# Optimization experiments

Measured on AMD Instinct MI355X. Metric: run time of the kernel, lower is better.

## Reference

```python
import jax, jax.numpy as jnp
import numpy as np

V, S, D, NL, DF, R, DG = 50257, 1024, 640, 16, 2560, 24, 256
PLU = R * (R - 1) // 2  # 276
OFFSETS = (1, 2, 4, 8, 16, 32, 64)
EPS = 1e-6
LN_EPS = 1e-5
II, JJ = np.triu_indices(R, k=1)  # matches torch.triu_indices(r, r, offset=1) ordering


def setup_inputs() -> dict:
    key = jax.random.key(0)
    ks = jax.random.split(key, 16)
    B, L = 4, 1024
    def n(k, shape):
        return jax.random.normal(k, shape, jnp.float32) * 0.02
    return {
        "input_ids": jax.random.randint(ks[0], (B, L), 0, V, jnp.int32),
        "tok_emb": n(ks[1], (V, D)),          # tied with lm_head
        "pos_emb": n(ks[2], (S, D)),
        "ln1_w": jnp.ones((NL, D)), "ln1_b": jnp.zeros((NL, D)),
        "red_w": n(ks[3], (NL, R, D)), "red_b": jnp.zeros((NL, R)),
        "gp1_w": n(ks[4], (NL, DG, PLU)), "gp1_b": jnp.zeros((NL, DG)),
        "gp2_w": n(ks[5], (NL, D, DG)), "gp2_b": jnp.zeros((NL, D)),
        "gate_w": n(ks[6], (NL, D, 2 * D)), "gate_b": jnp.zeros((NL, D)),
        "ln2_w": jnp.ones((NL, D)), "ln2_b": jnp.zeros((NL, D)),
        "fc1_w": n(ks[7], (NL, DF, D)), "fc1_b": jnp.zeros((NL, DF)),
        "fc2_w": n(ks[8], (NL, D, DF)), "fc2_b": jnp.zeros((NL, D)),
        "fn_w": jnp.ones((D,)), "fn_b": jnp.zeros((D,)),
    }


def _ln(x, w, b):
    m = jnp.mean(x, -1, keepdims=True)
    v = jnp.mean((x - m) ** 2, -1, keepdims=True)
    return (x - m) / jnp.sqrt(v + LN_EPS) * w + b


def _forward(input_ids, tok_emb, pos_emb, ln1_w, ln1_b, red_w, red_b,
             gp1_w, gp1_b, gp2_w, gp2_b, gate_w, gate_b,
             ln2_w, ln2_b, fc1_w, fc1_b, fc2_w, fc2_b, fn_w, fn_b):
    B, L = input_ids.shape
    x = tok_emb[input_ids] + pos_emb[jnp.arange(L)][None]  # (B,L,D), dropout=0 (eval)
    for l in range(NL):
        # --- CausalGrassmannMixer ---
        h = _ln(x, ln1_w[l], ln1_b[l])
        z = jnp.einsum('bld,rd->blr', h, red_w[l]) + red_b[l]  # (B,L,R)
        geom_sum = jnp.zeros_like(h)
        count = jnp.zeros((B, L, 1), h.dtype)
        for delta in OFFSETS:
            if delta >= L:
                continue
            z_past = jnp.pad(z[:, :L - delta], ((0, 0), (delta, 0), (0, 0)))
            # Plucker coordinates, normalized
            p = z_past[..., II] * z[..., JJ] - z_past[..., JJ] * z[..., II]  # (B,L,PLU)
            norm = jnp.maximum(jnp.sqrt(jnp.sum(p * p, -1, keepdims=True)), EPS)
            p = p / norm
            g = jax.nn.gelu(jnp.einsum('blp,gp->blg', p, gp1_w[l]) + gp1_b[l], approximate=False)
            g = jnp.einsum('blg,dg->bld', g, gp2_w[l]) + gp2_b[l]
            mask = (jnp.arange(L) >= delta).astype(h.dtype)[None, :, None]
            geom_sum = geom_sum + g * mask
            count = count + mask
        g = geom_sum / jnp.maximum(count, 1.0)
        alpha = jax.nn.sigmoid(
            jnp.einsum('ble,de->bld', jnp.concatenate([h, g], -1), gate_w[l]) + gate_b[l])
        x = x + alpha * h + (1.0 - alpha) * g
        # --- FeedForward ---
        h2 = _ln(x, ln2_w[l], ln2_b[l])
        ff = jax.nn.gelu(jnp.einsum('bld,fd->blf', h2, fc1_w[l]) + fc1_b[l], approximate=False)
        x = x + jnp.einsum('blf,df->bld', ff, fc2_w[l]) + fc2_b[l]
    x = _ln(x, fn_w, fn_b)
    return jnp.einsum('bld,vd->blv', x, tok_emb)  # tied lm_head


def reference(input_ids, tok_emb, pos_emb, ln1_w, ln1_b, red_w, red_b,
              gp1_w, gp1_b, gp2_w, gp2_b, gate_w, gate_b,
              ln2_w, ln2_b, fc1_w, fc1_b, fc2_w, fc2_b, fn_w, fn_b):
    return _forward(input_ids, tok_emb, pos_emb, ln1_w, ln1_b, red_w, red_b,
                    gp1_w, gp1_b, gp2_w, gp2_b, gate_w, gate_b,
                    ln2_w, ln2_b, fc1_w, fc1_b, fc2_w, fc2_b, fn_w, fn_b)
```

## Files before the change

kernel.cpp:

```cpp
#include <hip/hip_runtime.h>
#include <cmath>

#define V_ 50257
#define D_ 640
#define NL_ 16
#define DF_ 2560
#define R_ 24
#define DG_ 256
#define PLU_ 276
#define PLUP_ 288
#define B_ 4
#define L_ 1024
#define M_ (B_*L_)
#define EPS_ 1e-6f
#define LN_EPS_ 1e-5f

typedef __bf16 bf16x8 __attribute__((ext_vector_type(8)));
typedef float f32x4 __attribute__((ext_vector_type(4)));

__device__ __forceinline__ float gelu_exact(float x) {
    return 0.5f * x * (1.0f + erff(x * 0.70710678118654752f));
}
__device__ __forceinline__ float sigmoid_f(float x) {
    return 1.0f / (1.0f + expf(-x));
}
__device__ __forceinline__ ushort f2b(float f) {
    union { float f; unsigned u; } v; v.f = f;
    unsigned u = v.u;
    return (ushort)((u + 0x7FFFu + ((u >> 16) & 1u)) >> 16);
}
__device__ __forceinline__ float b2f(ushort b) {
    union { unsigned u; float f; } v; v.u = ((unsigned)b) << 16;
    return v.f;
}

#define GLOAD16(gptr, lptr) \
    __builtin_amdgcn_global_load_lds((const __attribute__((address_space(1))) void*)(gptr), \
                                     (__attribute__((address_space(3))) void*)(lptr), 16, 0, 0)


#define AS_(b) (shmem + (b) * 4096)
#define BS_(b) (shmem + 8192 + (b) * 4096)
#define STAGE128(b, k0) do { \
    GLOAD16(A + (size_t)(bm + w * 32 + srow) * (size_t)K + ((k0) + scol), AS_(b) + (w * 32) * 32); \
    GLOAD16(A + (size_t)(bm + w * 32 + 16 + srow) * (size_t)K + ((k0) + scol), AS_(b) + (w * 32 + 16) * 32); \
    int rb0_ = bn + w * 32 + srow;      if (rb0_ > N - 1) rb0_ = N - 1; \
    int rb1_ = bn + w * 32 + 16 + srow; if (rb1_ > N - 1) rb1_ = N - 1; \
    GLOAD16(W + (size_t)rb0_ * (size_t)K + ((k0) + scol), BS_(b) + (w * 32) * 32); \
    GLOAD16(W + (size_t)rb1_ * (size_t)K + ((k0) + scol), BS_(b) + (w * 32 + 16) * 32); \
} while (0)

template<int EPI>
__global__ __launch_bounds__(256) void mgemm128_k(
    const ushort* __restrict__ A, const ushort* __restrict__ W,
    const float* __restrict__ bias, float* __restrict__ Cf,
    ushort* __restrict__ Cb, int M, int N, int K)
{
    __shared__ ushort shmem[16384];
    const int tid = threadIdx.x;
    const int lane = tid & 63;
    const int w = tid >> 6;
    const int wr = w >> 1, wc = w & 1;
    const int lr = lane & 15, lk = lane >> 4;
    const int bm = blockIdx.x * 128, bn = blockIdx.y * 128;
    const int srow = lane >> 2;
    const int scol = (((lane & 3) ^ ((srow >> 1) & 3)) * 8);

    f32x4 acc[4][4] = {};
    const int nt = K >> 5;

    STAGE128(0, 0);
    asm volatile("s_waitcnt vmcnt(0)" ::: "memory");
    __builtin_amdgcn_s_barrier();

    int cur = 0;
    for (int t = 0; t < nt; ++t) {
        if (t + 1 < nt) { STAGE128(cur ^ 1, (t + 1) * 32); }
        bf16x8 af[4], bfr[4];
        #pragma unroll
        for (int m = 0; m < 4; ++m) {
            int rr = wr * 64 + m * 16 + lr;
            af[m] = *reinterpret_cast<const bf16x8*>(&AS_(cur)[rr * 32 + ((lk ^ ((rr >> 1) & 3)) * 8)]);
        }
        #pragma unroll
        for (int n = 0; n < 4; ++n) {
            int rr = wc * 64 + n * 16 + lr;
            bfr[n] = *reinterpret_cast<const bf16x8*>(&BS_(cur)[rr * 32 + ((lk ^ ((rr >> 1) & 3)) * 8)]);
        }
        #pragma unroll
        for (int m = 0; m < 4; ++m)
            #pragma unroll
            for (int n = 0; n < 4; ++n)
                acc[m][n] = __builtin_amdgcn_mfma_f32_16x16x32_bf16(af[m], bfr[n], acc[m][n], 0, 0, 0);
        asm volatile("s_waitcnt vmcnt(0)" ::: "memory");
        __builtin_amdgcn_s_barrier();
        cur ^= 1;
    }

    #pragma unroll
    for (int n = 0; n < 4; ++n) {
        int col = bn + wc * 64 + n * 16 + lr;
        if (col >= N) continue;
        float bsv = bias ? bias[col] : 0.0f;
        #pragma unroll
        for (int m = 0; m < 4; ++m) {
            #pragma unroll
            for (int r4 = 0; r4 < 4; ++r4) {
                int row = bm + wr * 64 + m * 16 + lk * 4 + r4;
                float o = acc[m][n][r4] + bsv;
                size_t idx = (size_t)row * N + col;
                if (EPI == 1) Cb[idx] = f2b(gelu_exact(o));
                else          Cb[idx] = f2b(o);
            }
        }
    }
}

#define AS2_(b) (shmem + (b) * 8192)
#define BS2_(b) (shmem + 16384 + (b) * 4096)
#define STAGE256(b, k0) do { \
    GLOAD16(A + (size_t)(bm + w * 32 + srow) * (size_t)K + ((k0) + scol), AS2_(b) + (w * 32) * 32); \
    GLOAD16(A + (size_t)(bm + w * 32 + 16 + srow) * (size_t)K + ((k0) + scol), AS2_(b) + (w * 32 + 16) * 32); \
    int rb_ = bn + w * 16 + srow; if (rb_ > N - 1) rb_ = N - 1; \
    GLOAD16(W + (size_t)rb_ * (size_t)K + ((k0) + scol), BS2_(b) + (w * 16) * 32); \
} while (0)

__global__ __launch_bounds__(512) void mgemm256nt_k(
    const ushort* __restrict__ A, const ushort* __restrict__ W,
    float* __restrict__ Cf, int M, int N, int K)
{
    __shared__ ushort shmem[24576];
    const int tid = threadIdx.x;
    const int lane = tid & 63;
    const int w = tid >> 6;
    const int wr = w >> 1, wc = w & 1;
    const int lr = lane & 15, lk = lane >> 4;
    const int bm = blockIdx.x * 256, bn = blockIdx.y * 128;
    const int srow = lane >> 2;
    const int scol = (((lane & 3) ^ ((srow >> 1) & 3)) * 8);

    f32x4 acc[4][4] = {};
    const int nt = K >> 5;

    STAGE256(0, 0);
    asm volatile("s_waitcnt vmcnt(0)" ::: "memory");
    __builtin_amdgcn_s_barrier();

    int cur = 0;
    for (int t = 0; t < nt; ++t) {
        if (t + 1 < nt) { STAGE256(cur ^ 1, (t + 1) * 32); }
        bf16x8 af[4], bfr[4];
        #pragma unroll
        for (int m = 0; m < 4; ++m) {
            int rr = wr * 64 + m * 16 + lr;
            af[m] = *reinterpret_cast<const bf16x8*>(&AS2_(cur)[rr * 32 + ((lk ^ ((rr >> 1) & 3)) * 8)]);
        }
        #pragma unroll
        for (int n = 0; n < 4; ++n) {
            int rr = wc * 64 + n * 16 + lr;
            bfr[n] = *reinterpret_cast<const bf16x8*>(&BS2_(cur)[rr * 32 + ((lk ^ ((rr >> 1) & 3)) * 8)]);
        }
        #pragma unroll
        for (int m = 0; m < 4; ++m)
            #pragma unroll
            for (int n = 0; n < 4; ++n)
                acc[m][n] = __builtin_amdgcn_mfma_f32_16x16x32_bf16(af[m], bfr[n], acc[m][n], 0, 0, 0);
        asm volatile("s_waitcnt vmcnt(0)" ::: "memory");
        __builtin_amdgcn_s_barrier();
        cur ^= 1;
    }

    float* lds_f = (float*)shmem;
    const int wbase = w * (16 * 68);
    #pragma unroll
    for (int m = 0; m < 4; ++m) {
        #pragma unroll
        for (int n = 0; n < 4; ++n) {
            #pragma unroll
            for (int r4 = 0; r4 < 4; ++r4)
                lds_f[wbase + (lk * 4 + r4) * 68 + n * 16 + lr] = acc[m][n][r4];
        }
        __syncthreads();
        #pragma unroll
        for (int r = 0; r < 16; ++r) {
            int row = bm + wr * 64 + m * 16 + r;
            int col = bn + wc * 64 + lane;
            float v = lds_f[wbase + r * 68 + lane];
            if (col < N)
                __builtin_nontemporal_store(v, &Cf[(size_t)row * N + col]);
        }
        __syncthreads();
    }
}

#define STAGE12864(b, k0) do { \
    GLOAD16(A + (size_t)(bm + w * 16 + srow) * (size_t)K + ((k0) + scol), &As[b][(w * 16) * 32]); \
    GLOAD16(A + (size_t)(bm + 64 + w * 16 + srow) * (size_t)K + ((k0) + scol), &As[b][(64 + w * 16) * 32]); \
    GLOAD16(W + (size_t)(bn + w * 16 + srow) * (size_t)K + ((k0) + scol), &Bs[b][(w * 16) * 32]); \
} while (0)

template<int EPI>
__global__ __launch_bounds__(256) void mgemm12864_k(
    const ushort* __restrict__ A, const ushort* __restrict__ W,
    const float* __restrict__ bias, float* __restrict__ Cf,
    const ushort* __restrict__ hg, ushort* __restrict__ ub,
    int M, int N, int K)
{
    __shared__ ushort As[2][128 * 32];
    __shared__ ushort Bs[2][64 * 32];
    const int tid = threadIdx.x;
    const int lane = tid & 63;
    const int w = tid >> 6;
    const int wr = w >> 1, wc = w & 1;
    const int lr = lane & 15, lk = lane >> 4;
    const int bm = blockIdx.x * 128, bn = blockIdx.y * 64;
    const int srow = lane >> 2;
    const int scol = (((lane & 3) ^ ((srow >> 1) & 3)) * 8);

    f32x4 acc[4][2] = {};
    const int nt = K >> 5;

    STAGE12864(0, 0);
    asm volatile("s_waitcnt vmcnt(0)" ::: "memory");
    __builtin_amdgcn_s_barrier();

    int cur = 0;
    for (int t = 0; t < nt; ++t) {
        if (t + 1 < nt) { STAGE12864(cur ^ 1, (t + 1) * 32); }
        bf16x8 af[4], bfr[2];
        #pragma unroll
        for (int m = 0; m < 4; ++m) {
            int rr = wr * 64 + m * 16 + lr;
            af[m] = *reinterpret_cast<const bf16x8*>(&As[cur][rr * 32 + ((lk ^ ((rr >> 1) & 3)) * 8)]);
        }
        #pragma unroll
        for (int n = 0; n < 2; ++n) {
            int rr = wc * 32 + n * 16 + lr;
            bfr[n] = *reinterpret_cast<const bf16x8*>(&Bs[cur][rr * 32 + ((lk ^ ((rr >> 1) & 3)) * 8)]);
        }
        #pragma unroll
        for (int m = 0; m < 4; ++m)
            #pragma unroll
            for (int n = 0; n < 2; ++n)
                acc[m][n] = __builtin_amdgcn_mfma_f32_16x16x32_bf16(af[m], bfr[n], acc[m][n], 0, 0, 0);
        asm volatile("s_waitcnt vmcnt(0)" ::: "memory");
        __builtin_amdgcn_s_barrier();
        cur ^= 1;
    }

    #pragma unroll
    for (int n = 0; n < 2; ++n) {
        int col = bn + wc * 32 + n * 16 + lr;
        float bsv = bias ? bias[col] : 0.0f;
        #pragma unroll
        for (int m = 0; m < 4; ++m) {
            #pragma unroll
            for (int r4 = 0; r4 < 4; ++r4) {
                int row = bm + wr * 64 + m * 16 + lk * 4 + r4;
                float o = acc[m][n][r4] + bsv;
                size_t idx = (size_t)row * N + col;
                if (EPI == 2) {
                    float a = sigmoid_f(o);
                    float hv = b2f(hg[(size_t)row * (2 * D_) + col]);
                    float gv = b2f(hg[(size_t)row * (2 * D_) + D_ + col]);
                    Cf[idx] = Cf[idx] + a * hv + (1.0f - a) * gv;
                } else if (EPI == 3) {
                    Cf[idx] += o;
                } else if (EPI == 5) {
                    if ((row & (L_ - 1)) == 0) o = 0.0f;
                    ub[(size_t)row * (2 * D_) + D_ + col] = f2b(o);
                }
            }
        }
    }
}

__global__ __launch_bounds__(256) void credsum_k(
    const ushort* __restrict__ c1b, ushort* __restrict__ crb)
{
    int idx4 = blockIdx.x * 256 + threadIdx.x;
    if (idx4 >= M_ * DG_ / 4) return;
    int idx = idx4 * 4;
    int row = idx / DG_;
    int l = row & (L_ - 1);
    float s0 = 0.f, s1 = 0.f, s2 = 0.f, s3 = 0.f;
    int c = 0;
    #pragma unroll
    for (int oi = 0; oi < 7; ++oi) {
        if (l >= (1 << oi)) {
            ushort4 v = *reinterpret_cast<const ushort4*>(c1b + (size_t)oi * M_ * DG_ + idx);
            s0 += b2f(v.x); s1 += b2f(v.y); s2 += b2f(v.z); s3 += b2f(v.w);
            ++c;
        }
    }
    float inv = 1.0f / (float)max(c, 1);
    ushort4 o;
    o.x = f2b(s0 * inv); o.y = f2b(s1 * inv); o.z = f2b(s2 * inv); o.w = f2b(s3 * inv);
    *reinterpret_cast<ushort4*>(crb + idx) = o;
}

__global__ __launch_bounds__(128) void lnred_k(
    const float* __restrict__ x, const float* __restrict__ w,
    const float* __restrict__ b, const float* __restrict__ rw,
    const float* __restrict__ rb, ushort* __restrict__ hgb,
    float* __restrict__ z)
{
    int row = blockIdx.x;
    int tid = threadIdx.x;
    const float* xr = x + (size_t)row * D_;
    __shared__ float hrow[D_];
    __shared__ float parts[R_][5];
    float v[5];
    float sum = 0.f, sumsq = 0.f;
    #pragma unroll
    for (int t = 0; t < 5; ++t) {
        v[t] = xr[tid + t * 128];
        sum += v[t]; sumsq += v[t] * v[t];
    }
    #pragma unroll
    for (int off = 32; off > 0; off >>= 1) {
        sum += __shfl_down(sum, off);
        sumsq += __shfl_down(sumsq, off);
    }
    __shared__ float s0[2], s1[2];
    if ((tid & 63) == 0) { s0[tid >> 6] = sum; s1[tid >> 6] = sumsq; }
    __syncthreads();
    float m = (s0[0] + s0[1]) * (1.0f / D_);
    float var = (s1[0] + s1[1]) * (1.0f / D_) - m * m;
    float inv = rsqrtf(var + LN_EPS_);
    #pragma unroll
    for (int t = 0; t < 5; ++t) {
        int d = tid + t * 128;
        float o = (v[t] - m) * inv * w[d] + b[d];
        hgb[(size_t)row * (2 * D_) + d] = f2b(o);
        hrow[d] = o;
    }
    __syncthreads();
    if (tid < 120) {
        int c = tid / 5, ch = tid - c * 5;
        const float4* hv = (const float4*)(hrow + ch * 128);
        const float4* wv = (const float4*)(rw + (size_t)c * D_ + ch * 128);
        float p = 0.f;
        #pragma unroll 8
        for (int k = 0; k < 32; ++k) {
            float4 a = hv[k], bb = wv[k];
            p += a.x * bb.x + a.y * bb.y + a.z * bb.z + a.w * bb.w;
        }
        parts[c][ch] = p;
    }
    __syncthreads();
    if (tid < R_) {
        float s = parts[tid][0] + parts[tid][1] + parts[tid][2] + parts[tid][3] + parts[tid][4];
        z[(size_t)row * R_ + tid] = s + rb[tid];
    }
}

__global__ __launch_bounds__(256) void embed_k(
    const int* __restrict__ ids, const float* __restrict__ tok,
    const float* __restrict__ pos, float* __restrict__ x)
{
    int idx = blockIdx.x * 256 + threadIdx.x;
    if (idx >= M_ * D_) return;
    int row = idx / D_;
    int d = idx - row * D_;
    int l = row & (L_ - 1);
    x[idx] = tok[(size_t)ids[row] * D_ + d] + pos[(size_t)l * D_ + d];
}

__global__ __launch_bounds__(256) void cvt_k(
    const float* __restrict__ src, ushort* __restrict__ dst, int n)
{
    int idx = blockIdx.x * 256 + threadIdx.x;
    if (idx < n) dst[idx] = f2b(src[idx]);
}

#define WC_G1  73728
#define WC_G2  (WC_G1 + 163840)
#define WC_GT  (WC_G2 + 819200)
#define WC_F1  (WC_GT + 1638400)
#define WC_F2  (WC_F1 + 1638400)
__device__ __forceinline__ void wconv_body(
    int idx, const float* g1, const float* g2, const float* gt,
    const float* f1, const float* f2, ushort* wb)
{
    if (idx < WC_G1) {
        int row = idx / PLUP_, c = idx - row * PLUP_;
        wb[idx] = (c < PLU_) ? f2b(g1[row * PLU_ + c]) : (ushort)0;
    } else if (idx < WC_G2) {
        wb[idx] = f2b(g2[idx - WC_G1]);
    } else if (idx < WC_GT) {
        wb[idx] = f2b(gt[idx - WC_G2]);
    } else if (idx < WC_F1) {
        wb[idx] = f2b(f1[idx - WC_GT]);
    } else if (idx < WC_F2) {
        wb[idx] = f2b(f2[idx - WC_F1]);
    }
}

__global__ __launch_bounds__(256) void wconv_k(
    const float* __restrict__ g1, const float* __restrict__ g2,
    const float* __restrict__ gt, const float* __restrict__ f1,
    const float* __restrict__ f2, ushort* __restrict__ wb)
{
    int idx = blockIdx.x * 256 + threadIdx.x;
    wconv_body(idx, g1, g2, gt, f1, f2, wb);
}

__global__ __launch_bounds__(256) void wconv_all_k(
    const float* __restrict__ g1, const float* __restrict__ g2,
    const float* __restrict__ gt, const float* __restrict__ f1,
    const float* __restrict__ f2, ushort* __restrict__ wb_all)
{
    int l = blockIdx.y;
    int idx = blockIdx.x * 256 + threadIdx.x;
    wconv_body(idx,
               g1 + (size_t)l * DG_ * PLU_, g2 + (size_t)l * D_ * DG_,
               gt + (size_t)l * D_ * 2 * D_, f1 + (size_t)l * DF_ * D_,
               f2 + (size_t)l * D_ * DF_, wb_all + (size_t)l * WC_F2);
}

__global__ __launch_bounds__(128) void ln_k(
    const float* __restrict__ x, const float* __restrict__ w,
    const float* __restrict__ b, float* __restrict__ outf,
    ushort* __restrict__ outb, int bstride)
{
    int row = blockIdx.x;
    int tid = threadIdx.x;
    const float* xr = x + (size_t)row * D_;
    float v[5];
    float sum = 0.f, sumsq = 0.f;
    #pragma unroll
    for (int t = 0; t < 5; ++t) {
        v[t] = xr[tid + t * 128];
        sum += v[t]; sumsq += v[t] * v[t];
    }
    #pragma unroll
    for (int off = 32; off > 0; off >>= 1) {
        sum += __shfl_down(sum, off);
        sumsq += __shfl_down(sumsq, off);
    }
    __shared__ float s0[2], s1[2];
    if ((tid & 63) == 0) { s0[tid >> 6] = sum; s1[tid >> 6] = sumsq; }
    __syncthreads();
    float m = (s0[0] + s0[1]) * (1.0f / D_);
    float var = (s1[0] + s1[1]) * (1.0f / D_) - m * m;
    float inv = rsqrtf(var + LN_EPS_);
    #pragma unroll
    for (int t = 0; t < 5; ++t) {
        int d = tid + t * 128;
        float o = (v[t] - m) * inv * w[d] + b[d];
        if (outf) outf[(size_t)row * D_ + d] = o;
        if (outb) outb[(size_t)row * bstride + d] = f2b(o);
    }
}

__global__ __launch_bounds__(128) void plucker7_k(
    const float* __restrict__ z, ushort* __restrict__ pb)
{
    int oi = blockIdx.y;
    int delta = 1 << oi;
    int row = blockIdx.x;
    int l = row & (L_ - 1);
    int tid = threadIdx.x;
    ushort* out = pb + ((size_t)oi * M_ + row) * PLUP_;
    if (l < delta) {
        for (int idx = tid; idx < PLUP_; idx += 128) out[idx] = 0;
        return;
    }
    __shared__ float zc[R_], zp[R_];
    if (tid < R_) {
        zc[tid] = z[(size_t)row * R_ + tid];
        zp[tid] = z[(size_t)(row - delta) * R_ + tid];
    }
    __syncthreads();
    float vals[3];
    float ss = 0.f;
    #pragma unroll
    for (int t = 0; t < 3; ++t) {
        int idx = tid + t * 128;
        float val = 0.f;
        if (idx < PLU_) {
            int i = 0, rem = idx;
            while (rem >= 23 - i) { rem -= 23 - i; ++i; }
            int j = i + 1 + rem;
            val = zp[i] * zc[j] - zp[j] * zc[i];
        }
        vals[t] = val;
        ss += val * val;
    }
    #pragma unroll
    for (int off = 32; off > 0; off >>= 1) ss += __shfl_down(ss, off);
    __shared__ float wsum[2];
    if ((tid & 63) == 0) wsum[tid >> 6] = ss;
    __syncthreads();
    float inv = 1.0f / fmaxf(sqrtf(wsum[0] + wsum[1]), EPS_);
    #pragma unroll
    for (int t = 0; t < 3; ++t) {
        int idx = tid + t * 128;
        if (idx < PLUP_) out[idx] = (idx < PLU_) ? f2b(vals[t] * inv) : (ushort)0;
    }
}

static void mg128(int epi, const ushort* A, const ushort* W, const float* bias,
                  float* Cf, ushort* Cb, int M, int N, int K, hipStream_t s)
{
    dim3 grid(M / 128, (N + 127) / 128), block(256);
    if (epi == 1) mgemm128_k<1><<<grid, block, 0, s>>>(A, W, bias, Cf, Cb, M, N, K);
    else          mgemm128_k<4><<<grid, block, 0, s>>>(A, W, bias, Cf, Cb, M, N, K);
}

static void mg12864(int epi, const ushort* A, const ushort* W, const float* bias,
                    float* Cf, const ushort* hg, ushort* ub,
                    int M, int N, int K, hipStream_t s)
{
    dim3 grid(M / 128, N / 64), block(256);
    if (epi == 2)      mgemm12864_k<2><<<grid, block, 0, s>>>(A, W, bias, Cf, hg, ub, M, N, K);
    else if (epi == 3) mgemm12864_k<3><<<grid, block, 0, s>>>(A, W, bias, Cf, hg, ub, M, N, K);
    else               mgemm12864_k<5><<<grid, block, 0, s>>>(A, W, bias, Cf, hg, ub, M, N, K);
}

extern "C" void kernel_launch(void* const* d_in, const int* in_sizes, int n_in,
                              void* d_out, int out_size, void* d_ws, size_t ws_size,
                              hipStream_t stream)
{
    const int*   ids   = (const int*)d_in[0];
    const float* tok   = (const float*)d_in[1];
    const float* pos   = (const float*)d_in[2];
    const float* ln1w  = (const float*)d_in[3];
    const float* ln1b  = (const float*)d_in[4];
    const float* redw  = (const float*)d_in[5];
    const float* redb  = (const float*)d_in[6];
    const float* gp1w  = (const float*)d_in[7];
    const float* gp1b  = (const float*)d_in[8];
    const float* gp2w  = (const float*)d_in[9];
    const float* gp2b  = (const float*)d_in[10];
    const float* gatew = (const float*)d_in[11];
    const float* gateb = (const float*)d_in[12];
    const float* ln2w  = (const float*)d_in[13];
    const float* ln2b  = (const float*)d_in[14];
    const float* fc1w  = (const float*)d_in[15];
    const float* fc1b  = (const float*)d_in[16];
    const float* fc2w  = (const float*)d_in[17];
    const float* fc2b  = (const float*)d_in[18];
    const float* fnw   = (const float*)d_in[19];
    const float* fnb   = (const float*)d_in[20];
    float* out = (float*)d_out;

    const size_t MD = (size_t)M_ * D_;
    float* ws = (float*)d_ws;
    float* x = ws;
    float* z = x + MD;
    ushort* pb    = (ushort*)(z + (size_t)M_ * R_);
    ushort* c1b   = pb + (size_t)7 * M_ * PLUP_;
    ushort* crb   = c1b + (size_t)7 * M_ * DG_;
    ushort* hgb   = crb + (size_t)M_ * DG_;
    ushort* h2b   = hgb + (size_t)M_ * 2 * D_;
    ushort* ffb   = h2b + MD;
    ushort* xnb   = ffb + (size_t)M_ * DF_;
    ushort* tokb  = xnb + MD;
    ushort* wb    = tokb + (size_t)V_ * D_;

    const size_t base_bytes = (size_t)((char*)wb - (char*)d_ws);
    const bool all_w = ws_size >= base_bytes + (size_t)NL_ * WC_F2 * 2;

    const int ELT_GRID = (M_ * D_ + 255) / 256;
    const int WC_GRID = (WC_F2 + 255) / 256;

    embed_k<<<ELT_GRID, 256, 0, stream>>>(ids, tok, pos, x);
    cvt_k<<<(V_ * D_ + 255) / 256, 256, 0, stream>>>(tok, tokb, V_ * D_);
    if (all_w)
        wconv_all_k<<<dim3(WC_GRID, NL_), 256, 0, stream>>>(gp1w, gp2w, gatew, fc1w, fc2w, wb);

    for (int l = 0; l < NL_; ++l) {
        const ushort* wbl = all_w ? wb + (size_t)l * WC_F2 : wb;
        if (!all_w)
            wconv_k<<<WC_GRID, 256, 0, stream>>>(
                gp1w + (size_t)l * DG_ * PLU_, gp2w + (size_t)l * D_ * DG_,
                gatew + (size_t)l * D_ * 2 * D_, fc1w + (size_t)l * DF_ * D_,
                fc2w + (size_t)l * D_ * DF_, wb);
        lnred_k<<<M_, 128, 0, stream>>>(x, ln1w + (size_t)l * D_, ln1b + (size_t)l * D_,
                                        redw + (size_t)l * R_ * D_, redb + (size_t)l * R_,
                                        hgb, z);
        plucker7_k<<<dim3(M_, 7), 128, 0, stream>>>(z, pb);
        mg128(1, pb, wbl, gp1b + (size_t)l * DG_, nullptr, c1b, 7 * M_, DG_, PLUP_, stream);
        credsum_k<<<(M_ * DG_ / 4 + 255) / 256, 256, 0, stream>>>(c1b, crb);
        mg12864(5, crb, wbl + WC_G1, gp2b + (size_t)l * D_, nullptr, hgb, hgb,
                M_, D_, DG_, stream);
        mg12864(2, hgb, wbl + WC_G2, gateb + (size_t)l * D_, x, hgb, nullptr,
                M_, D_, 2 * D_, stream);
        ln_k<<<M_, 128, 0, stream>>>(x, ln2w + (size_t)l * D_, ln2b + (size_t)l * D_,
                                     nullptr, h2b, D_);
        mg128(1, h2b, wbl + WC_GT, fc1b + (size_t)l * DF_, nullptr, ffb, M_, DF_, D_, stream);
        mg12864(3, ffb, wbl + WC_F1, fc2b + (size_t)l * D_, x, nullptr, nullptr,
                M_, D_, DF_, stream);
    }
    ln_k<<<M_, 128, 0, stream>>>(x, fnw, fnb, nullptr, xnb, D_);
    {
        dim3 grid(M_ / 256, (V_ + 127) / 128), block(512);
        mgemm256nt_k<<<grid, block, 0, stream>>>(xnb, tokb, out, M_, V_, D_);
    }
}
```

Baseline: 4.047 ms.

## Vectorize elementwise kernels, merge Plucker offsets per row, retile first grassmann GEMM

Embedding, token-table conversion and weight conversion kernels now process float4 per thread with ushort4 stores, cutting instruction and transaction count. The seven per-offset Plucker blocks are merged into one block per row that loops over offsets and reuses the current-row z in shared memory. The gp1 GEMM moves from the 128-tile kernel to the 128x64 kernel with a new GELU epilogue and a column bound check. This adds extra barriers in the Plucker loop and relies on K=288 fitting the 128x64 kernel's K stepping.

```diff
diff --git a/kernel.cpp b/kernel.cpp
--- a/kernel.cpp
+++ b/kernel.cpp
@@ -33,6 +33,11 @@
     union { unsigned u; float f; } v; v.u = ((unsigned)b) << 16;
     return v.f;
 }
+__device__ __forceinline__ ushort4 f4b4(float4 v) {
+    ushort4 o;
+    o.x = f2b(v.x); o.y = f2b(v.y); o.z = f2b(v.z); o.w = f2b(v.w);
+    return o;
+}
 
 #define GLOAD16(gptr, lptr) \
     __builtin_amdgcn_global_load_lds((const __attribute__((address_space(1))) void*)(gptr), \
@@ -251,6 +256,7 @@
     #pragma unroll
     for (int n = 0; n < 2; ++n) {
         int col = bn + wc * 32 + n * 16 + lr;
+        if (col >= N) continue;
         float bsv = bias ? bias[col] : 0.0f;
         #pragma unroll
         for (int m = 0; m < 4; ++m) {
@@ -259,7 +265,9 @@
                 int row = bm + wr * 64 + m * 16 + lk * 4 + r4;
                 float o = acc[m][n][r4] + bsv;
                 size_t idx = (size_t)row * N + col;
-                if (EPI == 2) {
+                if (EPI == 1) {
+                    ub[idx] = f2b(gelu_exact(o));
+                } else if (EPI == 2) {
                     float a = sigmoid_f(o);
                     float hv = b2f(hg[(size_t)row * (2 * D_) + col]);
                     float gv = b2f(hg[(size_t)row * (2 * D_) + D_ + col]);
@@ -355,23 +363,78 @@
     }
 }
 
+__global__ __launch_bounds__(128) void plucker_all_k(
+    const float* __restrict__ z, ushort* __restrict__ pb)
+{
+    int row = blockIdx.x;
+    int l = row & (L_ - 1);
+    int tid = threadIdx.x;
+    __shared__ float zc[R_], zp[R_];
+    __shared__ float wsum[2];
+    if (tid < R_) zc[tid] = z[(size_t)row * R_ + tid];
+    for (int oi = 0; oi < 7; ++oi) {
+        int delta = 1 << oi;
+        ushort* out = pb + ((size_t)oi * M_ + row) * PLUP_;
+        if (l < delta) {
+            __syncthreads();
+            for (int idx = tid; idx < PLUP_; idx += 128) out[idx] = 0;
+            __syncthreads();
+            continue;
+        }
+        if (tid < R_) zp[tid] = z[(size_t)(row - delta) * R_ + tid];
+        __syncthreads();
+        float vals[3];
+        float ss = 0.f;
+        #pragma unroll
+        for (int t = 0; t < 3; ++t) {
+            int idx = tid + t * 128;
+            float val = 0.f;
+            if (idx < PLU_) {
+                int i = 0, rem = idx;
+                while (rem >= 23 - i) { rem -= 23 - i; ++i; }
+                int j = i + 1 + rem;
+                val = zp[i] * zc[j] - zp[j] * zc[i];
+            }
+            vals[t] = val;
+            ss += val * val;
+        }
+        #pragma unroll
+        for (int off = 32; off > 0; off >>= 1) ss += __shfl_down(ss, off);
+        if ((tid & 63) == 0) wsum[tid >> 6] = ss;
+        __syncthreads();
+        float inv = 1.0f / fmaxf(sqrtf(wsum[0] + wsum[1]), EPS_);
+        #pragma unroll
+        for (int t = 0; t < 3; ++t) {
+            int idx = tid + t * 128;
+            if (idx < PLUP_) out[idx] = (idx < PLU_) ? f2b(vals[t] * inv) : (ushort)0;
+        }
+        __syncthreads();
+    }
+}
+
 __global__ __launch_bounds__(256) void embed_k(
     const int* __restrict__ ids, const float* __restrict__ tok,
     const float* __restrict__ pos, float* __restrict__ x)
 {
-    int idx = blockIdx.x * 256 + threadIdx.x;
-    if (idx >= M_ * D_) return;
+    int idx4 = blockIdx.x * 256 + threadIdx.x;
+    if (idx4 >= M_ * D_ / 4) return;
+    int idx = idx4 * 4;
     int row = idx / D_;
     int d = idx - row * D_;
     int l = row & (L_ - 1);
-    x[idx] = tok[(size_t)ids[row] * D_ + d] + pos[(size_t)l * D_ + d];
+    float4 t = *reinterpret_cast<const float4*>(tok + (size_t)ids[row] * D_ + d);
+    float4 p = *reinterpret_cast<const float4*>(pos + (size_t)l * D_ + d);
+    float4 o = make_float4(t.x + p.x, t.y + p.y, t.z + p.z, t.w + p.w);
+    *reinterpret_cast<float4*>(x + idx) = o;
 }
 
 __global__ __launch_bounds__(256) void cvt_k(
-    const float* __restrict__ src, ushort* __restrict__ dst, int n)
-{
-    int idx = blockIdx.x * 256 + threadIdx.x;
-    if (idx < n) dst[idx] = f2b(src[idx]);
+    const float* __restrict__ src, ushort* __restrict__ dst, int n4)
+{
+    int idx4 = blockIdx.x * 256 + threadIdx.x;
+    if (idx4 >= n4) return;
+    float4 v = *reinterpret_cast<const float4*>(src + idx4 * 4);
+    *reinterpret_cast<ushort4*>(dst + idx4 * 4) = f4b4(v);
 }
 
 #define WC_G1  73728
@@ -379,44 +442,32 @@
 #define WC_GT  (WC_G2 + 819200)
 #define WC_F1  (WC_GT + 1638400)
 #define WC_F2  (WC_F1 + 1638400)
-__device__ __forceinline__ void wconv_body(
-    int idx, const float* g1, const float* g2, const float* gt,
-    const float* f1, const float* f2, ushort* wb)
-{
-    if (idx < WC_G1) {
-        int row = idx / PLUP_, c = idx - row * PLUP_;
-        wb[idx] = (c < PLU_) ? f2b(g1[row * PLU_ + c]) : (ushort)0;
-    } else if (idx < WC_G2) {
-        wb[idx] = f2b(g2[idx - WC_G1]);
-    } else if (idx < WC_GT) {
-        wb[idx] = f2b(gt[idx - WC_G2]);
-    } else if (idx < WC_F1) {
-        wb[idx] = f2b(f1[idx - WC_GT]);
-    } else if (idx < WC_F2) {
-        wb[idx] = f2b(f2[idx - WC_F1]);
-    }
-}
-
-__global__ __launch_bounds__(256) void wconv_k(
-    const float* __restrict__ g1, const float* __restrict__ g2,
-    const float* __restrict__ gt, const float* __restrict__ f1,
-    const float* __restrict__ f2, ushort* __restrict__ wb)
-{
-    int idx = blockIdx.x * 256 + threadIdx.x;
-    wconv_body(idx, g1, g2, gt, f1, f2, wb);
-}
-
 __global__ __launch_bounds__(256) void wconv_all_k(
     const float* __restrict__ g1, const float* __restrict__ g2,
     const float* __restrict__ gt, const float* __restrict__ f1,
     const float* __restrict__ f2, ushort* __restrict__ wb_all)
 {
     int l = blockIdx.y;
-    int idx = blockIdx.x * 256 + threadIdx.x;
-    wconv_body(idx,
-               g1 + (size_t)l * DG_ * PLU_, g2 + (size_t)l * D_ * DG_,
-               gt + (size_t)l * D_ * 2 * D_, f1 + (size_t)l * DF_ * D_,
-               f2 + (size_t)l * D_ * DF_, wb_all + (size_t)l * WC_F2);
+    int idx4 = blockIdx.x * 256 + threadIdx.x;
+    int idx = idx4 * 4;
+    if (idx >= WC_F2) return;
+    ushort* wb = wb_all + (size_t)l * WC_F2;
+    float4 v;
+    if (idx < WC_G1) {
+        const float* s = g1 + (size_t)l * DG_ * PLU_;
+        int row = idx / PLUP_, c = idx - row * PLUP_;
+        if (c < PLU_) v = *reinterpret_cast<const float4*>(s + (size_t)row * PLU_ + c);
+        else          v = make_float4(0.f, 0.f, 0.f, 0.f);
+    } else if (idx < WC_G2) {
+        v = *reinterpret_cast<const float4*>(g2 + (size_t)l * D_ * DG_ + (idx - WC_G1));
+    } else if (idx < WC_GT) {
+        v = *reinterpret_cast<const float4*>(gt + (size_t)l * D_ * 2 * D_ + (idx - WC_G2));
+    } else if (idx < WC_F1) {
+        v = *reinterpret_cast<const float4*>(f1 + (size_t)l * DF_ * D_ + (idx - WC_GT));
+    } else {
+        v = *reinterpret_cast<const float4*>(f2 + (size_t)l * D_ * DF_ + (idx - WC_F1));
+    }
+    *reinterpret_cast<ushort4*>(wb + idx) = f4b4(v);
 }
 
 __global__ __launch_bounds__(128) void ln_k(
@@ -454,53 +505,6 @@
     }
 }
 
-__global__ __launch_bounds__(128) void plucker7_k(
-    const float* __restrict__ z, ushort* __restrict__ pb)
-{
-    int oi = blockIdx.y;
-    int delta = 1 << oi;
-    int row = blockIdx.x;
-    int l = row & (L_ - 1);
-    int tid = threadIdx.x;
-    ushort* out = pb + ((size_t)oi * M_ + row) * PLUP_;
-    if (l < delta) {
-        for (int idx = tid; idx < PLUP_; idx += 128) out[idx] = 0;
-        return;
-    }
-    __shared__ float zc[R_], zp[R_];
-    if (tid < R_) {
-        zc[tid] = z[(size_t)row * R_ + tid];
-        zp[tid] = z[(size_t)(row - delta) * R_ + tid];
-    }
-    __syncthreads();
-    float vals[3];
-    float ss = 0.f;
-    #pragma unroll
-    for (int t = 0; t < 3; ++t) {
-        int idx = tid + t * 128;
-        float val = 0.f;
-        if (idx < PLU_) {
-            int i = 0, rem = idx;
-            while (rem >= 23 - i) { rem -= 23 - i; ++i; }
-            int j = i + 1 + rem;
-            val = zp[i] * zc[j] - zp[j] * zc[i];
-        }
-        vals[t] = val;
-        ss += val * val;
-    }
-    #pragma unroll
-    for (int off = 32; off > 0; off >>= 1) ss += __shfl_down(ss, off);
-    __shared__ float wsum[2];
-    if ((tid & 63) == 0) wsum[tid >> 6] = ss;
-    __syncthreads();
-    float inv = 1.0f / fmaxf(sqrtf(wsum[0] + wsum[1]), EPS_);
-    #pragma unroll
-    for (int t = 0; t < 3; ++t) {
-        int idx = tid + t * 128;
-        if (idx < PLUP_) out[idx] = (idx < PLU_) ? f2b(vals[t] * inv) : (ushort)0;
-    }
-}
-
 static void mg128(int epi, const ushort* A, const ushort* W, const float* bias,
                   float* Cf, ushort* Cb, int M, int N, int K, hipStream_t s)
 {
@@ -514,7 +518,8 @@
                     int M, int N, int K, hipStream_t s)
 {
     dim3 grid(M / 128, N / 64), block(256);
-    if (epi == 2)      mgemm12864_k<2><<<grid, block, 0, s>>>(A, W, bias, Cf, hg, ub, M, N, K);
+    if (epi == 1)      mgemm12864_k<1><<<grid, block, 0, s>>>(A, W, bias, Cf, hg, ub, M, N, K);
+    else if (epi == 2) mgemm12864_k<2><<<grid, block, 0, s>>>(A, W, bias, Cf, hg, ub, M, N, K);
     else if (epi == 3) mgemm12864_k<3><<<grid, block, 0, s>>>(A, W, bias, Cf, hg, ub, M, N, K);
     else               mgemm12864_k<5><<<grid, block, 0, s>>>(A, W, bias, Cf, hg, ub, M, N, K);
 }
@@ -563,26 +568,26 @@
     const size_t base_bytes = (size_t)((char*)wb - (char*)d_ws);
     const bool all_w = ws_size >= base_bytes + (size_t)NL_ * WC_F2 * 2;
 
-    const int ELT_GRID = (M_ * D_ + 255) / 256;
-    const int WC_GRID = (WC_F2 + 255) / 256;
-
-    embed_k<<<ELT_GRID, 256, 0, stream>>>(ids, tok, pos, x);
-    cvt_k<<<(V_ * D_ + 255) / 256, 256, 0, stream>>>(tok, tokb, V_ * D_);
+    const int WC_GRID4 = (WC_F2 / 4 + 255) / 256;
+
+    embed_k<<<(M_ * D_ / 4 + 255) / 256, 256, 0, stream>>>(ids, tok, pos, x);
+    cvt_k<<<(V_ * D_ / 4 + 255) / 256, 256, 0, stream>>>(tok, tokb, V_ * D_ / 4);
     if (all_w)
-        wconv_all_k<<<dim3(WC_GRID, NL_), 256, 0, stream>>>(gp1w, gp2w, gatew, fc1w, fc2w, wb);
+        wconv_all_k<<<dim3(WC_GRID4, NL_), 256, 0, stream>>>(gp1w, gp2w, gatew, fc1w, fc2w, wb);
 
     for (int l = 0; l < NL_; ++l) {
         const ushort* wbl = all_w ? wb + (size_t)l * WC_F2 : wb;
         if (!all_w)
-            wconv_k<<<WC_GRID, 256, 0, stream>>>(
+            wconv_all_k<<<dim3(WC_GRID4, 1), 256, 0, stream>>>(
                 gp1w + (size_t)l * DG_ * PLU_, gp2w + (size_t)l * D_ * DG_,
                 gatew + (size_t)l * D_ * 2 * D_, fc1w + (size_t)l * DF_ * D_,
                 fc2w + (size_t)l * D_ * DF_, wb);
         lnred_k<<<M_, 128, 0, stream>>>(x, ln1w + (size_t)l * D_, ln1b + (size_t)l * D_,
                                         redw + (size_t)l * R_ * D_, redb + (size_t)l * R_,
                                         hgb, z);
-        plucker7_k<<<dim3(M_, 7), 128, 0, stream>>>(z, pb);
-        mg128(1, pb, wbl, gp1b + (size_t)l * DG_, nullptr, c1b, 7 * M_, DG_, PLUP_, stream);
+        plucker_all_k<<<M_, 128, 0, stream>>>(z, pb);
+        mg12864(1, pb, wbl, gp1b + (size_t)l * DG_, nullptr, nullptr, c1b,
+                7 * M_, DG_, PLUP_, stream);
         credsum_k<<<(M_ * DG_ / 4 + 255) / 256, 256, 0, stream>>>(c1b, crb);
         mg12864(5, crb, wbl + WC_G1, gp2b + (size_t)l * D_, nullptr, hgb, hgb,
                 M_, D_, DG_, stream);
```

After: 3.972 ms. About the same (-1.9%).
